# Performance work log

Hardware: AMD Instinct MI355X
Metric: run time of the kernel (lower is better)

Reference implementation:

```python
import jax, jax.numpy as jnp
import numpy as np

BETA_MIN = 0.1
BETA_MAX = 20.0


def _Beta(t):
    # integral of linear beta schedule
    return BETA_MIN * t + 0.5 * (BETA_MAX - BETA_MIN) * t ** 2


def setup_inputs() -> dict:
    key = jax.random.key(0)
    k1, k2, k3, k4, k5 = jax.random.split(key, 5)
    B, K, D = 4096, 128, 256
    x = jax.random.normal(k1, (B, D), dtype=jnp.float32)
    t = jax.random.uniform(k2, (B,), dtype=jnp.float32)
    centers = jax.random.normal(k3, (K, D), dtype=jnp.float32)
    # keep stds positive and well-conditioned
    stds = 0.5 + 0.5 * jax.random.uniform(k4, (K, D), dtype=jnp.float32)
    # positive mixture weights (original only requires positivity, takes log)
    weights = 0.1 + jax.random.uniform(k5, (K,), dtype=jnp.float32)
    return {"x": x, "t": t, "centers": centers, "stds": stds, "weights": weights}


def reference(x, t, centers, stds, weights):
    ndim = centers.shape[1]

    def log_prob(xx):
        Bt = _Beta(t)[:, None, None]                 # [B,1,1]
        a = jnp.exp(-Bt / 2)
        centers_t = a * centers[None]                # [B,K,D]
        var_t = jnp.exp(-Bt) * stds[None] ** 2 + 1.0 - jnp.exp(-Bt)  # [B,K,D]
        diff = xx[:, None, :] - centers_t            # [B,K,D]
        # NOTE: faithful to source, which uses ndim/2 * sum(log(2*pi*var)) (not 1/2)
        lp = (-(diff ** 2) / (2.0 * var_t)).sum(-1) \
             - (ndim / 2) * jnp.log(2.0 * jnp.pi * var_t).sum(-1)    # [B,K]
        lp = lp + jnp.log(weights)[None, :]
        return jax.scipy.special.logsumexp(lp, axis=1)               # [B]

    grad_log_prob = jax.grad(lambda xx: log_prob(xx).sum())(x)       # [B,D]
    Bt = _Beta(t)[:, None]                                           # [B,1]
    return -jnp.sqrt(1.0 - jnp.exp(-Bt)) * grad_log_prob
```

## Files before the change

kernel.cpp:

```cpp
#include <hip/hip_runtime.h>
#include <math.h>


constexpr int Kc = 128;
constexpr int Dc = 256;
constexpr int G  = 4;

typedef float f2 __attribute__((ext_vector_type(2)));
typedef float f4 __attribute__((ext_vector_type(4)));

static __device__ __forceinline__ f2 fma2(f2 a, f2 b, f2 c) {
    return __builtin_elementwise_fma(a, b, c);
}
static __device__ __forceinline__ f2 splat2(float s) { return (f2){s, s}; }

__global__ void prep_kernel(const float* __restrict__ centers,
                            const float* __restrict__ stds,
                            float* __restrict__ CA8, f2* __restrict__ P2) {
    int idx = blockIdx.x * blockDim.x + threadIdx.x;
    if (idx >= Kc * Dc) return;
    int k = idx >> 8;
    int d = idx & (Dc - 1);
    float c = centers[idx];
    float s = stds[idx];
    float A = s * s - 1.0f;
    int o = (d >> 2) * (Kc * 8) + k * 8 + (d & 3);
    CA8[o]     = c;
    CA8[o + 4] = A;
    P2[idx] = (f2){c, A};
}

__global__ __launch_bounds__(512, 8) void score_kernel(
    const float* __restrict__ x, const float* __restrict__ t,
    const float* __restrict__ weights,
    const float* __restrict__ CA8, const f2* __restrict__ P2,
    float* __restrict__ out)
{
    const int b0  = blockIdx.x * G;
    const int tid = threadIdx.x;

    __shared__ __align__(16) float xT[Dc][G];
    __shared__ float part1[G][4][Kc];
    __shared__ float partL[G][4][Kc];
    __shared__ __align__(16) float peT[Kc][G];
    __shared__ float wmax[G][2];
    __shared__ float wsum[G][2];
    __shared__ __align__(16) float Opart[G][Dc];

    float e[G], na[G], sg[G];
    #pragma unroll
    for (int g = 0; g < G; ++g) {
        float tt = t[b0 + g];
        float Bt = fmaf(9.95f * tt, tt, 0.1f * tt);
        float ee = __expf(-Bt);
        e[g]  = ee;
        na[g] = -sqrtf(ee);
        sg[g] = sqrtf(1.0f - ee);
    }
    f2 e2[2]  = {{e[0], e[1]}, {e[2], e[3]}};
    f2 na2[2] = {{na[0], na[1]}, {na[2], na[3]}};
    const f2 one2 = {1.0f, 1.0f};

    {
        const int dd = tid & (Dc - 1);
        const int gh = tid >> 8;
        xT[dd][gh]     = x[(b0 + gh) * Dc + dd];
        xT[dd][gh + 2] = x[(b0 + gh + 2) * Dc + dd];
    }
    __syncthreads();

    const int kk      = tid & (Kc - 1);
    const int quarter = tid >> 7;
    const int dbase   = quarter * (Dc / 4);

    const f4* xTv = (const f4*)(&xT[0][0]);

    f2 acc1[2] = {{0.f, 0.f}, {0.f, 0.f}};
    float accL[G] = {0.f, 0.f, 0.f, 0.f};

    for (int grp = 0; grp < 4; ++grp) {
        f2 prod[2] = {{1.f, 1.f}, {1.f, 1.f}};
        #pragma unroll
        for (int q = 0; q < 4; ++q) {
            const int d0 = dbase + (grp * 4 + q) * 4;
            const float* base = CA8 + ((size_t)(d0 >> 2) * Kc + kk) * 8;
            f4 c4 = *(const f4*)base;
            f4 A4 = *(const f4*)(base + 4);
            f4 xv0 = xTv[d0 + 0];
            f4 xv1 = xTv[d0 + 1];
            f4 xv2 = xTv[d0 + 2];
            f4 xv3 = xTv[d0 + 3];
            #pragma unroll
            for (int p = 0; p < 2; ++p) {
                f2 ep = e2[p], nap = na2[p];
                f2 x0 = {xv0[2*p], xv0[2*p+1]};
                f2 x1 = {xv1[2*p], xv1[2*p+1]};
                f2 x2 = {xv2[2*p], xv2[2*p+1]};
                f2 x3 = {xv3[2*p], xv3[2*p+1]};
                f2 v0 = fma2(ep, splat2(A4[0]), one2);
                f2 v1 = fma2(ep, splat2(A4[1]), one2);
                f2 v2 = fma2(ep, splat2(A4[2]), one2);
                f2 v3 = fma2(ep, splat2(A4[3]), one2);
                f2 f0 = fma2(nap, splat2(c4[0]), x0);
                f2 f1 = fma2(nap, splat2(c4[1]), x1);
                f2 f2_ = fma2(nap, splat2(c4[2]), x2);
                f2 f3 = fma2(nap, splat2(c4[3]), x3);
                f2 s0 = f0 * f0, s1 = f1 * f1, s2 = f2_ * f2_, s3 = f3 * f3;
                f2 d01 = v0 * v1, d23 = v2 * v3;
                f2 n01 = fma2(s1, v0, s0 * v1);
                f2 n23 = fma2(s3, v2, s2 * v3);
                f2 den = d01 * d23;
                f2 num = fma2(n23, d01, n01 * d23);
                f2 r = {__builtin_amdgcn_rcpf(den[0]),
                        __builtin_amdgcn_rcpf(den[1])};
                acc1[p] = fma2(num, r, acc1[p]);
                prod[p] = prod[p] * den;
            }
        }
        accL[0] += __log2f(prod[0][0]);
        accL[1] += __log2f(prod[0][1]);
        accL[2] += __log2f(prod[1][0]);
        accL[3] += __log2f(prod[1][1]);
    }
    #pragma unroll
    for (int p = 0; p < 2; ++p) {
        part1[2*p  ][quarter][kk] = acc1[p][0];
        part1[2*p+1][quarter][kk] = acc1[p][1];
    }
    #pragma unroll
    for (int g = 0; g < G; ++g)
        partL[g][quarter][kk] = accL[g];
    __syncthreads();

    float lpv[G];
    if (tid < Kc) {
        float lw = __logf(weights[tid]);
        #pragma unroll
        for (int g = 0; g < G; ++g) {
            float S1 = (part1[g][0][tid] + part1[g][1][tid])
                     + (part1[g][2][tid] + part1[g][3][tid]);
            float S2 = (partL[g][0][tid] + partL[g][1][tid])
                     + (partL[g][2][tid] + partL[g][3][tid]);
            lpv[g] = fmaf(-0.5f, S1, fmaf(-88.72283911167299f, S2, lw));
            float m = lpv[g];
            #pragma unroll
            for (int off = 32; off > 0; off >>= 1)
                m = fmaxf(m, __shfl_xor(m, off, 64));
            if ((tid & 63) == 0) wmax[g][tid >> 6] = m;
        }
    }
    __syncthreads();
    if (tid < Kc) {
        #pragma unroll
        for (int g = 0; g < G; ++g) {
            float m  = fmaxf(wmax[g][0], wmax[g][1]);
            float pe = __expf(lpv[g] - m);
            peT[tid][g] = pe;
            float s = pe;
            #pragma unroll
            for (int off = 32; off > 0; off >>= 1)
                s += __shfl_xor(s, off, 64);
            if ((tid & 63) == 0) wsum[g][tid >> 6] = s;
        }
    }
    __syncthreads();

    const int dd    = tid & (Dc - 1);
    const int khalf = tid >> 8;
    f4 xvv = xTv[dd];
    f2 xp[2] = {{xvv[0], xvv[1]}, {xvv[2], xvv[3]}};
    f2 O[2] = {{0.f, 0.f}, {0.f, 0.f}};
    const f4* peTv = (const f4*)(&peT[0][0]);
    const f2* pp = P2 + dd;

    const int kq0 = khalf * 16;
    for (int kq = kq0; kq < kq0 + 16; ++kq) {
        const int k0 = kq * 4;
        f2 ca0 = pp[(k0 + 0) * Dc];
        f2 ca1 = pp[(k0 + 1) * Dc];
        f2 ca2 = pp[(k0 + 2) * Dc];
        f2 ca3 = pp[(k0 + 3) * Dc];
        f4 p0 = peTv[k0 + 0];
        f4 p1 = peTv[k0 + 1];
        f4 p2 = peTv[k0 + 2];
        f4 p3 = peTv[k0 + 3];
        #pragma unroll
        for (int p = 0; p < 2; ++p) {
            f2 ep = e2[p], nap = na2[p];
            f2 v0 = fma2(ep, splat2(ca0[1]), one2);
            f2 v1 = fma2(ep, splat2(ca1[1]), one2);
            f2 v2 = fma2(ep, splat2(ca2[1]), one2);
            f2 v3 = fma2(ep, splat2(ca3[1]), one2);
            f2 f0 = fma2(nap, splat2(ca0[0]), xp[p]);
            f2 f1 = fma2(nap, splat2(ca1[0]), xp[p]);
            f2 f2_ = fma2(nap, splat2(ca2[0]), xp[p]);
            f2 f3 = fma2(nap, splat2(ca3[0]), xp[p]);
            f2 u0 = (f2){p0[2*p], p0[2*p+1]} * f0;
            f2 u1 = (f2){p1[2*p], p1[2*p+1]} * f1;
            f2 u2 = (f2){p2[2*p], p2[2*p+1]} * f2_;
            f2 u3 = (f2){p3[2*p], p3[2*p+1]} * f3;
            f2 d01 = v0 * v1, d23 = v2 * v3;
            f2 n01 = fma2(u1, v0, u0 * v1);
            f2 n23 = fma2(u3, v2, u2 * v3);
            f2 den = d01 * d23;
            f2 num = fma2(n23, d01, n01 * d23);
            f2 r = {__builtin_amdgcn_rcpf(den[0]),
                    __builtin_amdgcn_rcpf(den[1])};
            O[p] = fma2(num, r, O[p]);
        }
    }

    if (khalf) {
        #pragma unroll
        for (int p = 0; p < 2; ++p) {
            #pragma unroll
            for (int j = 0; j < 2; ++j)
                Opart[2*p + j][dd] = O[p][j];
        }
    }
    __syncthreads();
    if (!khalf) {
        #pragma unroll
        for (int p = 0; p < 2; ++p) {
            #pragma unroll
            for (int j = 0; j < 2; ++j) {
                int g = 2 * p + j;
                float Z  = wsum[g][0] + wsum[g][1];
                float Ov = O[p][j] + Opart[g][dd];
                out[(b0 + g) * Dc + dd] = sg[g] * __builtin_amdgcn_rcpf(Z) * Ov;
            }
        }
    }
}

extern "C" void kernel_launch(void* const* d_in, const int* in_sizes, int n_in,
                              void* d_out, int out_size, void* d_ws, size_t ws_size,
                              hipStream_t stream) {
    const float* x       = (const float*)d_in[0];
    const float* t       = (const float*)d_in[1];
    const float* centers = (const float*)d_in[2];
    const float* stds    = (const float*)d_in[3];
    const float* weights = (const float*)d_in[4];
    float* outp = (float*)d_out;

    float* CA8 = (float*)d_ws;
    f2*    P2  = (f2*)(CA8 + Kc * Dc * 2);

    const int B = in_sizes[1];

    prep_kernel<<<(Kc * Dc + 255) / 256, 256, 0, stream>>>(centers, stds, CA8, P2);
    score_kernel<<<B / G, 512, 0, stream>>>(x, t, weights, CA8, P2, outp);
}
```

Baseline: 105.3 us.

## Software-prefetch center/variance loads with register double buffering in both loops

Splits the interleaved center/variance buffer into two separate planar arrays, each coalesced with f4 loads. Both the log-prob loop and the gradient loop now load the next group's parameters into a second register buffer while computing on the current one. Launch bounds drop from 8 to 4 waves per SIMD so the extra live registers fit. The aim is to hide global/L2 latency, at the cost of lower occupancy and possible register pressure.

After: 112.0 us. +6.3%, slower.

```diff
diff --git a/kernel.cpp b/kernel.cpp
--- a/kernel.cpp
+++ b/kernel.cpp
@@ -16,7 +16,8 @@
 
 __global__ void prep_kernel(const float* __restrict__ centers,
                             const float* __restrict__ stds,
-                            float* __restrict__ CA8, f2* __restrict__ P2) {
+                            float* __restrict__ C4, float* __restrict__ A4,
+                            f2* __restrict__ P2) {
     int idx = blockIdx.x * blockDim.x + threadIdx.x;
     if (idx >= Kc * Dc) return;
     int k = idx >> 8;
@@ -24,16 +25,17 @@
     float c = centers[idx];
     float s = stds[idx];
     float A = s * s - 1.0f;
-    int o = (d >> 2) * (Kc * 8) + k * 8 + (d & 3);
-    CA8[o]     = c;
-    CA8[o + 4] = A;
+    int o = ((d >> 2) * Kc + k) * 4 + (d & 3);
+    C4[o] = c;
+    A4[o] = A;
     P2[idx] = (f2){c, A};
 }
 
-__global__ __launch_bounds__(512, 8) void score_kernel(
+__global__ __launch_bounds__(512, 4) void score_kernel(
     const float* __restrict__ x, const float* __restrict__ t,
     const float* __restrict__ weights,
-    const float* __restrict__ CA8, const f2* __restrict__ P2,
+    const float* __restrict__ C4, const float* __restrict__ A4g,
+    const f2* __restrict__ P2,
     float* __restrict__ out)
 {
     const int b0  = blockIdx.x * G;
@@ -78,14 +80,33 @@
     f2 acc1[2] = {{0.f, 0.f}, {0.f, 0.f}};
     float accL[G] = {0.f, 0.f, 0.f, 0.f};
 
+    f4 cb[2][4], ab[2][4];
+    #pragma unroll
+    for (int q = 0; q < 4; ++q) {
+        const int d0 = dbase + q * 4;
+        const size_t ix = ((size_t)(d0 >> 2) * Kc + kk) * 4;
+        cb[0][q] = *(const f4*)(C4  + ix);
+        ab[0][q] = *(const f4*)(A4g + ix);
+    }
+
+    #pragma unroll 2
     for (int grp = 0; grp < 4; ++grp) {
+        const int cur = grp & 1;
+        const int nxt = cur ^ 1;
+        const int gN  = (grp + 1) & 3;
+        #pragma unroll
+        for (int q = 0; q < 4; ++q) {
+            const int d0n = dbase + (gN * 4 + q) * 4;
+            const size_t ix = ((size_t)(d0n >> 2) * Kc + kk) * 4;
+            cb[nxt][q] = *(const f4*)(C4  + ix);
+            ab[nxt][q] = *(const f4*)(A4g + ix);
+        }
         f2 prod[2] = {{1.f, 1.f}, {1.f, 1.f}};
         #pragma unroll
         for (int q = 0; q < 4; ++q) {
             const int d0 = dbase + (grp * 4 + q) * 4;
-            const float* base = CA8 + ((size_t)(d0 >> 2) * Kc + kk) * 8;
-            f4 c4 = *(const f4*)base;
-            f4 A4 = *(const f4*)(base + 4);
+            f4 c4 = cb[cur][q];
+            f4 A4 = ab[cur][q];
             f4 xv0 = xTv[d0 + 0];
             f4 xv1 = xTv[d0 + 1];
             f4 xv2 = xTv[d0 + 2];
@@ -174,12 +195,25 @@
     const f2* pp = P2 + dd;
 
     const int kq0 = khalf * 16;
+
+    f2 c2b[2][4];
+    #pragma unroll
+    for (int i = 0; i < 4; ++i)
+        c2b[0][i] = pp[(kq0 * 4 + i) * Dc];
+
+    #pragma unroll 2
     for (int kq = kq0; kq < kq0 + 16; ++kq) {
+        const int cur = kq & 1;
+        const int nxt = cur ^ 1;
+        const int k0n = ((kq + 1) * 4) & (Kc - 1);
+        #pragma unroll
+        for (int i = 0; i < 4; ++i)
+            c2b[nxt][i] = pp[(k0n + i) * Dc];
         const int k0 = kq * 4;
-        f2 ca0 = pp[(k0 + 0) * Dc];
-        f2 ca1 = pp[(k0 + 1) * Dc];
-        f2 ca2 = pp[(k0 + 2) * Dc];
-        f2 ca3 = pp[(k0 + 3) * Dc];
+        f2 ca0 = c2b[cur][0];
+        f2 ca1 = c2b[cur][1];
+        f2 ca2 = c2b[cur][2];
+        f2 ca3 = c2b[cur][3];
         f4 p0 = peTv[k0 + 0];
         f4 p1 = peTv[k0 + 1];
         f4 p2 = peTv[k0 + 2];
@@ -243,11 +277,12 @@
     const float* weights = (const float*)d_in[4];
     float* outp = (float*)d_out;
 
-    float* CA8 = (float*)d_ws;
-    f2*    P2  = (f2*)(CA8 + Kc * Dc * 2);
+    float* C4 = (float*)d_ws;
+    float* A4 = C4 + Kc * Dc;
+    f2*    P2 = (f2*)(A4 + Kc * Dc);
 
     const int B = in_sizes[1];
 
-    prep_kernel<<<(Kc * Dc + 255) / 256, 256, 0, stream>>>(centers, stds, CA8, P2);
-    score_kernel<<<B / G, 512, 0, stream>>>(x, t, weights, CA8, P2, outp);
-}
+    prep_kernel<<<(Kc * Dc + 255) / 256, 256, 0, stream>>>(centers, stds, C4, A4, P2);
+    score_kernel<<<B / G, 512, 0, stream>>>(x, t, weights, C4, A4, P2, outp);
+}
```
